# Performance work log

Measured on AMD Instinct MI355X. Metric: run time of the kernel, lower is better.

The kernel has to match this reference:

```python
import jax, jax.numpy as jnp
import numpy as np

DEPTH = 5  # init kwarg


def setup_inputs() -> dict:
    key = jax.random.key(0)
    ks = jax.random.split(key, 10)
    n_atoms, n_bonds, hidden, n_mols = 80000, 160001, 448, 4000
    ATOM_DIM, BOND_DIM = 38, 11
    inp = {
        "fatoms": jax.random.normal(ks[0], (n_atoms, ATOM_DIM), jnp.float32),
        "fbonds": jax.random.normal(ks[1], (n_bonds, ATOM_DIM + BOND_DIM), jnp.float32),
        "W_i": jax.random.normal(ks[2], (ATOM_DIM + BOND_DIM, hidden), jnp.float32) * 0.1,
        "W_h": jax.random.normal(ks[3], (hidden, hidden), jnp.float32) * 0.05,
        "W_o": jax.random.normal(ks[4], (ATOM_DIM + hidden, hidden), jnp.float32) * 0.05,
        "b_o": jax.random.normal(ks[5], (hidden,), jnp.float32),
        "agraph": jax.random.randint(ks[6], (n_atoms, 6), 0, n_bonds, jnp.int64),
        "bgraph": jax.random.randint(ks[7], (n_bonds, 6), 0, n_bonds, jnp.int64),
        "mol_idx": jnp.sort(jax.random.randint(ks[8], (n_atoms,), 0, n_mols, jnp.int64)),
        "n_mols": n_mols,
    }
    return inp


def reference(fatoms, fbonds, W_i, W_h, W_o, b_o, agraph, bgraph, mol_idx, n_mols):
    # binput: [n_bonds, hidden]
    binput = fbonds @ W_i
    message = jax.nn.relu(binput)
    for _ in range(DEPTH - 1):
        # padded-neighbor gather-sum over MAX_NB=6, then linear + relu
        nei = jnp.take(message, bgraph, axis=0).sum(axis=1)  # [n_bonds, hidden]
        message = jax.nn.relu(binput + nei @ W_h)
    # atom readout
    nei = jnp.take(message, agraph, axis=0).sum(axis=1)  # [n_atoms, hidden]
    ainput = jnp.concatenate([fatoms, nei], axis=1)
    atom_hiddens = jax.nn.relu(ainput @ W_o + b_o)
    # per-molecule mean pooling (scope -> segment ids)
    sums = jax.ops.segment_sum(atom_hiddens, mol_idx, num_segments=n_mols)
    counts = jax.ops.segment_sum(jnp.ones((atom_hiddens.shape[0],), atom_hiddens.dtype), mol_idx, num_segments=n_mols)
    return sums / jnp.maximum(counts, 1.0)[:, None]
```

## Files before the change

### kernel.cpp

```cpp
#include <hip/hip_runtime.h>

#define HIDDEN 448

typedef __attribute__((ext_vector_type(8))) short short8;
typedef __attribute__((ext_vector_type(4))) float f32x4;

__device__ __forceinline__ unsigned short f2bf(float f) {
    unsigned int u = __float_as_uint(f);
    u = (u + 0x7fffu + ((u >> 16) & 1u)) >> 16;
    return (unsigned short)u;
}
__device__ __forceinline__ float bf2f(unsigned short h) {
    return __uint_as_float(((unsigned int)h) << 16);
}
__device__ __forceinline__ unsigned int cvt_pk_bf16(float a, float b) {
    unsigned int r;
    asm("v_cvt_pk_bf16_f32 %0, %1, %2" : "=v"(r) : "v"(a), "v"(b));
    return r;
}
__device__ __forceinline__ void async16(void* lds, const void* g) {
    __builtin_amdgcn_global_load_lds(
        (const __attribute__((address_space(1))) unsigned int*)g,
        (__attribute__((address_space(3))) unsigned int*)lds, 16, 0, 0);
}

__global__ __launch_bounds__(256) void prep_wcat_kernel(
    const float* __restrict__ Wtop, int Ktop, const float* __restrict__ Wbot,
    unsigned short* __restrict__ out)
{
    const int idx = blockIdx.x * 256 + threadIdx.x;
    if (idx >= 448 * 512) return;
    const int n = idx >> 9, k = idx & 511;
    float v = 0.0f;
    if (k < Ktop) v = Wtop[k * HIDDEN + n];
    else if (k >= 64) v = Wbot[(k - 64) * HIDDEN + n];
    out[(size_t)n * 512 + (k ^ (((n >> 1) & 3) << 3))] = f2bf(v);
}

__global__ __launch_bounds__(256) void prep_apad_kernel(
    const float* __restrict__ A, int K, unsigned short* __restrict__ out,
    int Mreal, int total)
{
    const int idx = blockIdx.x * 256 + threadIdx.x;
    if (idx >= total) return;
    const int row = idx >> 6, k = idx & 63;
    const float v = (row < Mreal && k < K) ? A[(size_t)row * K + k] : 0.0f;
    out[(size_t)row * 64 + (k ^ (((row >> 1) & 3) << 3))] = f2bf(v);
}

template<int GRAPH, int OUTQ>
__global__ __launch_bounds__(512, 4) void gemm_mfma_kernel(
    const unsigned short* __restrict__ Apad,
    const unsigned char* __restrict__ Xq,
    const float* __restrict__ Xs,
    const int* __restrict__ graph,
    const unsigned short* __restrict__ BT,
    const float* __restrict__ bias,
    unsigned short* outh,
    unsigned char* __restrict__ outq,
    float* __restrict__ outs,
    int M, int nsteps)
{
    __shared__ __align__(16) unsigned char smem[37888];
    unsigned short* As = (unsigned short*)smem;
    unsigned short* Bs = (unsigned short*)(smem + 8192);
    float* rmaxbuf = (float*)(smem + 36864);

    const int tid = threadIdx.x, lane = tid & 63, wv = tid >> 6;
    const int row0 = blockIdx.x * 64;
    const int wrow = (wv & 1) * 32;
    const int wcol = (wv >> 1) * 112;
    const int rr = lane & 15, ch = lane >> 4;
    const int lrow = lane >> 2, lq = lane & 3;

    const int arow = tid >> 3, asub = tid & 7;
    const int ahh = asub >> 2, ac = asub & 3;
    const int awoff = arow * 64 + ahh * 32 + ((ac ^ ((arow >> 1) & 3)) << 3);

    int goff[6]; float gscl[6]; uint2 pf[6]; uint4 wreg;
    if (GRAPH) {
        const int grow = row0 + arow;
        const bool ok = grow < M;
        #pragma unroll
        for (int j = 0; j < 6; ++j) {
            const int gj = ok ? graph[(size_t)grow * 6 + j] : 0;
            goff[j] = gj * 448;
            gscl[j] = ok ? Xs[gj] : 0.0f;
        }
    }

    f32x4 acc[2][7] = {};

    for (int s = 0; s < nsteps; ++s) {
        if (GRAPH && s >= 2 && !(s & 1))
            *(uint4*)&As[awoff] = wreg;
        #pragma unroll
        for (int i = 0; i < 4; ++i) {
            const int t = wv + 8 * i;
            if (t < 28)
                async16(Bs + t * 512 + lane * 8,
                        BT + (size_t)(t * 16 + lrow) * 512 + s * 32 + lq * 8);
        }
        if (s == 0)
            async16(As + wv * 512 + lane * 8,
                    Apad + (size_t)(row0 + wv * 8) * 64 + lane * 8);
        __syncthreads();

        if (GRAPH && !(s & 1) && s <= 12) {
            const int pb = (s >> 1) * 64;
            #pragma unroll
            for (int j = 0; j < 6; ++j)
                pf[j] = *(const uint2*)(Xq + goff[j] + pb + asub * 8);
        }

        const int hoff = (s & 1) * 32;
        short8 av[2], bv[7];
        #pragma unroll
        for (int m = 0; m < 2; ++m) {
            const int r = wrow + m * 16 + rr;
            av[m] = *(const short8*)&As[r * 64 + hoff + ((ch ^ ((r >> 1) & 3)) << 3)];
        }
        #pragma unroll
        for (int n = 0; n < 7; ++n) {
            const int cl = wcol + n * 16 + rr;
            bv[n] = *(const short8*)&Bs[cl * 32 + ((ch ^ ((cl >> 1) & 3)) << 3)];
        }
        #pragma unroll
        for (int n = 0; n < 7; ++n)
            #pragma unroll
            for (int m = 0; m < 2; ++m)
                acc[m][n] = __builtin_amdgcn_mfma_f32_16x16x32_bf16(
                    av[m], bv[n], acc[m][n], 0, 0, 0);

        if (GRAPH && (s & 1) && s <= 13) {
            float a0 = 0, a1 = 0, a2 = 0, a3 = 0, a4 = 0, a5 = 0, a6 = 0, a7 = 0;
            #pragma unroll
            for (int j = 0; j < 6; ++j) {
                const uint2 b = pf[j];
                const float sc = gscl[j];
                a0 += (float)(b.x & 255u) * sc;
                a1 += (float)((b.x >> 8) & 255u) * sc;
                a2 += (float)((b.x >> 16) & 255u) * sc;
                a3 += (float)(b.x >> 24) * sc;
                a4 += (float)(b.y & 255u) * sc;
                a5 += (float)((b.y >> 8) & 255u) * sc;
                a6 += (float)((b.y >> 16) & 255u) * sc;
                a7 += (float)(b.y >> 24) * sc;
            }
            wreg.x = cvt_pk_bf16(a0, a1);
            wreg.y = cvt_pk_bf16(a2, a3);
            wreg.z = cvt_pk_bf16(a4, a5);
            wreg.w = cvt_pk_bf16(a6, a7);
        }
        __syncthreads();
    }

    const int r4 = ch << 2;

    if (OUTQ) {
        float rpm[2][4];
        #pragma unroll
        for (int m = 0; m < 2; ++m)
            #pragma unroll
            for (int j = 0; j < 4; ++j) {
                float mx = 0.0f;
                #pragma unroll
                for (int n = 0; n < 7; ++n) mx = fmaxf(mx, acc[m][n][j]);
                rpm[m][j] = mx;
            }
        #pragma unroll
        for (int off = 1; off < 16; off <<= 1)
            #pragma unroll
            for (int m = 0; m < 2; ++m)
                #pragma unroll
                for (int j = 0; j < 4; ++j)
                    rpm[m][j] = fmaxf(rpm[m][j], __shfl_xor(rpm[m][j], off));
        if (rr == 0)
            #pragma unroll
            for (int m = 0; m < 2; ++m)
                #pragma unroll
                for (int j = 0; j < 4; ++j)
                    rmaxbuf[(wrow + m * 16 + r4 + j) * 4 + (wv >> 1)] = rpm[m][j];
        __syncthreads();
        float inv[2][4];
        #pragma unroll
        for (int m = 0; m < 2; ++m)
            #pragma unroll
            for (int j = 0; j < 4; ++j) {
                const int rl = wrow + m * 16 + r4 + j;
                const float mx = fmaxf(fmaxf(rmaxbuf[rl * 4 + 0], rmaxbuf[rl * 4 + 1]),
                                       fmaxf(rmaxbuf[rl * 4 + 2], rmaxbuf[rl * 4 + 3]));
                inv[m][j] = (mx > 0.0f) ? (255.0f / mx) : 0.0f;
                if (wv < 2 && rr == 0 && row0 + rl < M)
                    outs[row0 + rl] = mx * (1.0f / 255.0f);
            }
        __syncthreads();
        unsigned char* q8 = smem;
        #pragma unroll
        for (int m = 0; m < 2; ++m)
            #pragma unroll
            for (int j = 0; j < 4; ++j) {
                const int rl = wrow + m * 16 + r4 + j;
                #pragma unroll
                for (int n = 0; n < 7; ++n) {
                    const float v = fmaxf(acc[m][n][j], 0.0f);
                    q8[rl * 448 + wcol + n * 16 + rr] =
                        (unsigned char)__float2uint_rn(fminf(v * inv[m][j], 255.0f));
                }
            }
        __syncthreads();
        #pragma unroll
        for (int i = 0; i < 4; ++i) {
            const int u = tid + 512 * i;
            if (u < 1792 && row0 + u / 28 < M)
                ((uint4*)(outq + (size_t)row0 * 448))[u] = ((const uint4*)q8)[u];
        }
    } else {
        #pragma unroll
        for (int n = 0; n < 7; ++n) {
            const int col = wcol + n * 16 + rr;
            const float bsv = bias ? bias[col] : 0.0f;
            #pragma unroll
            for (int m = 0; m < 2; ++m)
                #pragma unroll
                for (int j = 0; j < 4; ++j) {
                    const int row = row0 + wrow + m * 16 + r4 + j;
                    if (row < M)
                        outh[(size_t)row * HIDDEN + col] =
                            f2bf(fmaxf(acc[m][n][j] + bsv, 0.0f));
                }
        }
    }
}

__global__ void segmean_kernel(
    const unsigned short* __restrict__ ah, const int* __restrict__ mol_idx,
    float* __restrict__ out, int n_atoms)
{
    const int m = blockIdx.x;
    const int c = threadIdx.x;
    int l = 0, r = n_atoms;
    while (l < r) { const int mid = (l + r) >> 1; if (mol_idx[mid] < m) l = mid + 1; else r = mid; }
    const int start = l;
    r = n_atoms;
    while (l < r) { const int mid = (l + r) >> 1; if (mol_idx[mid] < m + 1) l = mid + 1; else r = mid; }
    const int end = l;
    float acc = 0.0f;
    for (int a = start; a < end; ++a) acc += bf2f(ah[(size_t)a * HIDDEN + c]);
    out[(size_t)m * HIDDEN + c] = acc / fmaxf((float)(end - start), 1.0f);
}

__global__ __launch_bounds__(256) void fill_kernel(float* __restrict__ out, int n, float val)
{
    const int i = blockIdx.x * 256 + threadIdx.x;
    if (i < n) out[i] = val;
}

extern "C" void kernel_launch(void* const* d_in, const int* in_sizes, int n_in,
                              void* d_out, int out_size, void* d_ws, size_t ws_size,
                              hipStream_t stream)
{
    const float* fatoms = (const float*)d_in[0];
    const float* fbonds = (const float*)d_in[1];
    const float* W_i    = (const float*)d_in[2];
    const float* W_h    = (const float*)d_in[3];
    const float* W_o    = (const float*)d_in[4];
    const float* b_o    = (const float*)d_in[5];
    const int*   agraph = (const int*)d_in[6];
    const int*   bgraph = (const int*)d_in[7];
    const int*   mol_idx= (const int*)d_in[8];

    const int n_atoms = in_sizes[0] / 38;
    const int n_bonds = in_sizes[1] / 49;
    const int n_mols  = out_size / HIDDEN;

    const int Mb_b = (n_bonds + 63) & ~63;
    const int Mb_a = (n_atoms + 63) & ~63;

    const size_t eW  = (size_t)448 * 512;
    const size_t eFb = (size_t)Mb_b * 64;
    const size_t eFa = (size_t)Mb_a * 64;
    const size_t eX  = (size_t)Mb_b * 448;

    const size_t need = 2 * eW * 2 + eFb * 2 + eFa * 2 +
                        2 * eX + 2 * (size_t)Mb_b * 4;

    const dim3 blk(256);

    if (ws_size >= need) {
        unsigned short* WhcatT  = (unsigned short*)d_ws;
        unsigned short* WocatT  = WhcatT + eW;
        unsigned short* fbondsP = WocatT + eW;
        unsigned short* fatomsP = fbondsP + eFb;
        unsigned char*  Xq0     = (unsigned char*)(fatomsP + eFa);
        unsigned char*  Xq1     = Xq0 + eX;
        float*          Xs0     = (float*)(Xq1 + eX);
        float*          Xs1     = Xs0 + Mb_b;

        const int wblocks = (448 * 512 + 255) / 256;
        hipLaunchKernelGGL(prep_wcat_kernel, dim3(wblocks), blk, 0, stream,
                           W_i, 49, W_h, WhcatT);
        hipLaunchKernelGGL(prep_wcat_kernel, dim3(wblocks), blk, 0, stream,
                           W_o, 38, W_o + 38 * HIDDEN, WocatT);
        hipLaunchKernelGGL(prep_apad_kernel, dim3(((int)eFb + 255) / 256), blk, 0, stream,
                           fbonds, 49, fbondsP, n_bonds, (int)eFb);
        hipLaunchKernelGGL(prep_apad_kernel, dim3(((int)eFa + 255) / 256), blk, 0, stream,
                           fatoms, 38, fatomsP, n_atoms, (int)eFa);

        const dim3 gB(Mb_b / 64), gA(Mb_a / 64), tpb(512);

        unsigned char* Xq[2] = {Xq0, Xq1};
        float*         Xs[2] = {Xs0, Xs1};

        hipLaunchKernelGGL((gemm_mfma_kernel<0, 1>), gB, tpb, 0, stream,
                           fbondsP, (const unsigned char*)nullptr, (const float*)nullptr,
                           (const int*)nullptr, WhcatT, (const float*)nullptr,
                           (unsigned short*)nullptr, Xq[0], Xs[0], n_bonds, 2);
        int p = 0;
        for (int it = 0; it < 4; ++it) {
            hipLaunchKernelGGL((gemm_mfma_kernel<1, 1>), gB, tpb, 0, stream,
                               fbondsP, Xq[p], Xs[p], bgraph, WhcatT,
                               (const float*)nullptr, (unsigned short*)nullptr,
                               Xq[p ^ 1], Xs[p ^ 1], n_bonds, 16);
            p ^= 1;
        }
        unsigned short* ah = (unsigned short*)Xq[p ^ 1];
        hipLaunchKernelGGL((gemm_mfma_kernel<1, 0>), gA, tpb, 0, stream,
                           fatomsP, Xq[p], Xs[p], agraph, WocatT, b_o,
                           ah, (unsigned char*)nullptr, (float*)nullptr, n_atoms, 16);
        hipLaunchKernelGGL(segmean_kernel, dim3(n_mols), dim3(HIDDEN), 0, stream,
                           ah, mol_idx, (float*)d_out, n_atoms);
    } else {
        const float val = -(float)((double)ws_size / (1024.0 * 1024.0));
        hipLaunchKernelGGL(fill_kernel, dim3((out_size + 255) / 256), blk, 0, stream,
                           (float*)d_out, out_size, val);
    }
}
```

Before: 1.014 ms.

## Fuse segment-mean pooling into readout GEMM epilogue via atomics

The atom readout GEMM epilogue now sums each thread's four rows per molecule and adds the result into the output with atomicAdd, instead of writing bf16 atom hiddens to memory. The segmean kernel becomes a simple normalization pass, and the output is zeroed with a memset first. The gather-reduce step is also moved from the end of an odd iteration to the start of the next even one, so the wreg carry register is no longer needed. This removes the intermediate write and re-read of the atom hidden states, at the cost of atomic contention and summation order that is no longer deterministic.

```diff
diff --git a/kernel.cpp b/kernel.cpp
--- a/kernel.cpp
+++ b/kernel.cpp
@@ -56,9 +56,10 @@
     const int* __restrict__ graph,
     const unsigned short* __restrict__ BT,
     const float* __restrict__ bias,
-    unsigned short* outh,
     unsigned char* __restrict__ outq,
     float* __restrict__ outs,
+    const int* __restrict__ molv,
+    float* __restrict__ dout,
     int M, int nsteps)
 {
     __shared__ __align__(16) unsigned char smem[37888];
@@ -75,9 +76,9 @@
 
     const int arow = tid >> 3, asub = tid & 7;
     const int ahh = asub >> 2, ac = asub & 3;
-    const int awoff = arow * 64 + ahh * 32 + ((ac ^ ((arow >> 1) & 3)) << 3);
-
-    int goff[6]; float gscl[6]; uint2 pf[6]; uint4 wreg;
+    const int awaddr = arow * 64 + ahh * 32 + ((ac ^ ((arow >> 1) & 3)) << 3);
+
+    int goff[6]; float gscl[6]; uint2 pf[6];
     if (GRAPH) {
         const int grow = row0 + arow;
         const bool ok = grow < M;
@@ -92,47 +93,7 @@
     f32x4 acc[2][7] = {};
 
     for (int s = 0; s < nsteps; ++s) {
-        if (GRAPH && s >= 2 && !(s & 1))
-            *(uint4*)&As[awoff] = wreg;
-        #pragma unroll
-        for (int i = 0; i < 4; ++i) {
-            const int t = wv + 8 * i;
-            if (t < 28)
-                async16(Bs + t * 512 + lane * 8,
-                        BT + (size_t)(t * 16 + lrow) * 512 + s * 32 + lq * 8);
-        }
-        if (s == 0)
-            async16(As + wv * 512 + lane * 8,
-                    Apad + (size_t)(row0 + wv * 8) * 64 + lane * 8);
-        __syncthreads();
-
-        if (GRAPH && !(s & 1) && s <= 12) {
-            const int pb = (s >> 1) * 64;
-            #pragma unroll
-            for (int j = 0; j < 6; ++j)
-                pf[j] = *(const uint2*)(Xq + goff[j] + pb + asub * 8);
-        }
-
-        const int hoff = (s & 1) * 32;
-        short8 av[2], bv[7];
-        #pragma unroll
-        for (int m = 0; m < 2; ++m) {
-            const int r = wrow + m * 16 + rr;
-            av[m] = *(const short8*)&As[r * 64 + hoff + ((ch ^ ((r >> 1) & 3)) << 3)];
-        }
-        #pragma unroll
-        for (int n = 0; n < 7; ++n) {
-            const int cl = wcol + n * 16 + rr;
-            bv[n] = *(const short8*)&Bs[cl * 32 + ((ch ^ ((cl >> 1) & 3)) << 3)];
-        }
-        #pragma unroll
-        for (int n = 0; n < 7; ++n)
-            #pragma unroll
-            for (int m = 0; m < 2; ++m)
-                acc[m][n] = __builtin_amdgcn_mfma_f32_16x16x32_bf16(
-                    av[m], bv[n], acc[m][n], 0, 0, 0);
-
-        if (GRAPH && (s & 1) && s <= 13) {
+        if (GRAPH && s >= 2 && !(s & 1)) {
             float a0 = 0, a1 = 0, a2 = 0, a3 = 0, a4 = 0, a5 = 0, a6 = 0, a7 = 0;
             #pragma unroll
             for (int j = 0; j < 6; ++j) {
@@ -147,11 +108,51 @@
                 a6 += (float)((b.y >> 16) & 255u) * sc;
                 a7 += (float)(b.y >> 24) * sc;
             }
-            wreg.x = cvt_pk_bf16(a0, a1);
-            wreg.y = cvt_pk_bf16(a2, a3);
-            wreg.z = cvt_pk_bf16(a4, a5);
-            wreg.w = cvt_pk_bf16(a6, a7);
-        }
+            uint4 w;
+            w.x = cvt_pk_bf16(a0, a1);
+            w.y = cvt_pk_bf16(a2, a3);
+            w.z = cvt_pk_bf16(a4, a5);
+            w.w = cvt_pk_bf16(a6, a7);
+            *(uint4*)&As[awaddr] = w;
+        }
+        #pragma unroll
+        for (int i = 0; i < 4; ++i) {
+            const int t = wv + 8 * i;
+            if (t < 28)
+                async16(Bs + t * 512 + lane * 8,
+                        BT + (size_t)(t * 16 + lrow) * 512 + s * 32 + lq * 8);
+        }
+        if (s == 0)
+            async16(As + wv * 512 + lane * 8,
+                    Apad + (size_t)(row0 + wv * 8) * 64 + lane * 8);
+        __syncthreads();
+
+        if (GRAPH && !(s & 1) && s <= 12) {
+            const int pb = (s >> 1) * 64;
+            #pragma unroll
+            for (int j = 0; j < 6; ++j)
+                pf[j] = *(const uint2*)(Xq + goff[j] + pb + asub * 8);
+        }
+
+        const int hoff = (s & 1) * 32;
+        short8 av[2], bv[7];
+        #pragma unroll
+        for (int m = 0; m < 2; ++m) {
+            const int r = wrow + m * 16 + rr;
+            av[m] = *(const short8*)&As[r * 64 + hoff + ((ch ^ ((r >> 1) & 3)) << 3)];
+        }
+        #pragma unroll
+        for (int n = 0; n < 7; ++n) {
+            const int cl = wcol + n * 16 + rr;
+            bv[n] = *(const short8*)&Bs[cl * 32 + ((ch ^ ((cl >> 1) & 3)) << 3)];
+        }
+        #pragma unroll
+        for (int n = 0; n < 7; ++n)
+            #pragma unroll
+            for (int m = 0; m < 2; ++m)
+                acc[m][n] = __builtin_amdgcn_mfma_f32_16x16x32_bf16(
+                    av[m], bv[n], acc[m][n], 0, 0, 0);
+
         __syncthreads();
     }
 
@@ -216,26 +217,45 @@
                 ((uint4*)(outq + (size_t)row0 * 448))[u] = ((const uint4*)q8)[u];
         }
     } else {
+        int mols[2][4];
+        #pragma unroll
+        for (int m = 0; m < 2; ++m)
+            #pragma unroll
+            for (int j = 0; j < 4; ++j) {
+                const int row = row0 + wrow + m * 16 + r4 + j;
+                mols[m][j] = (row < M) ? molv[row] : -1;
+            }
         #pragma unroll
         for (int n = 0; n < 7; ++n) {
             const int col = wcol + n * 16 + rr;
             const float bsv = bias ? bias[col] : 0.0f;
             #pragma unroll
-            for (int m = 0; m < 2; ++m)
+            for (int m = 0; m < 2; ++m) {
+                int curmol = -1;
+                float rs = 0.0f;
                 #pragma unroll
                 for (int j = 0; j < 4; ++j) {
-                    const int row = row0 + wrow + m * 16 + r4 + j;
-                    if (row < M)
-                        outh[(size_t)row * HIDDEN + col] =
-                            f2bf(fmaxf(acc[m][n][j] + bsv, 0.0f));
+                    if (mols[m][j] >= 0) {
+                        const float v = fmaxf(acc[m][n][j] + bsv, 0.0f);
+                        if (mols[m][j] != curmol) {
+                            if (curmol >= 0)
+                                atomicAdd(dout + (size_t)curmol * HIDDEN + col, rs);
+                            curmol = mols[m][j];
+                            rs = v;
+                        } else {
+                            rs += v;
+                        }
+                    }
                 }
+                if (curmol >= 0)
+                    atomicAdd(dout + (size_t)curmol * HIDDEN + col, rs);
+            }
         }
     }
 }
 
-__global__ void segmean_kernel(
-    const unsigned short* __restrict__ ah, const int* __restrict__ mol_idx,
-    float* __restrict__ out, int n_atoms)
+__global__ void norm_kernel(float* __restrict__ out,
+                            const int* __restrict__ mol_idx, int n_atoms)
 {
     const int m = blockIdx.x;
     const int c = threadIdx.x;
@@ -244,10 +264,7 @@
     const int start = l;
     r = n_atoms;
     while (l < r) { const int mid = (l + r) >> 1; if (mol_idx[mid] < m + 1) l = mid + 1; else r = mid; }
-    const int end = l;
-    float acc = 0.0f;
-    for (int a = start; a < end; ++a) acc += bf2f(ah[(size_t)a * HIDDEN + c]);
-    out[(size_t)m * HIDDEN + c] = acc / fmaxf((float)(end - start), 1.0f);
+    out[(size_t)m * HIDDEN + c] /= fmaxf((float)(l - start), 1.0f);
 }
 
 __global__ __launch_bounds__(256) void fill_kernel(float* __restrict__ out, int n, float val)
@@ -297,6 +314,8 @@
         float*          Xs0     = (float*)(Xq1 + eX);
         float*          Xs1     = Xs0 + Mb_b;
 
+        hipMemsetAsync(d_out, 0, (size_t)out_size * sizeof(float), stream);
+
         const int wblocks = (448 * 512 + 255) / 256;
         hipLaunchKernelGGL(prep_wcat_kernel, dim3(wblocks), blk, 0, stream,
                            W_i, 49, W_h, WhcatT);
@@ -315,21 +334,23 @@
         hipLaunchKernelGGL((gemm_mfma_kernel<0, 1>), gB, tpb, 0, stream,
                            fbondsP, (const unsigned char*)nullptr, (const float*)nullptr,
                            (const int*)nullptr, WhcatT, (const float*)nullptr,
-                           (unsigned short*)nullptr, Xq[0], Xs[0], n_bonds, 2);
+                           Xq[0], Xs[0], (const int*)nullptr, (float*)nullptr,
+                           n_bonds, 2);
         int p = 0;
         for (int it = 0; it < 4; ++it) {
             hipLaunchKernelGGL((gemm_mfma_kernel<1, 1>), gB, tpb, 0, stream,
                                fbondsP, Xq[p], Xs[p], bgraph, WhcatT,
-                               (const float*)nullptr, (unsigned short*)nullptr,
-                               Xq[p ^ 1], Xs[p ^ 1], n_bonds, 16);
+                               (const float*)nullptr,
+                               Xq[p ^ 1], Xs[p ^ 1], (const int*)nullptr,
+                               (float*)nullptr, n_bonds, 16);
             p ^= 1;
         }
-        unsigned short* ah = (unsigned short*)Xq[p ^ 1];
         hipLaunchKernelGGL((gemm_mfma_kernel<1, 0>), gA, tpb, 0, stream,
                            fatomsP, Xq[p], Xs[p], agraph, WocatT, b_o,
-                           ah, (unsigned char*)nullptr, (float*)nullptr, n_atoms, 16);
-        hipLaunchKernelGGL(segmean_kernel, dim3(n_mols), dim3(HIDDEN), 0, stream,
-                           ah, mol_idx, (float*)d_out, n_atoms);
+                           (unsigned char*)nullptr, (float*)nullptr,
+                           mol_idx, (float*)d_out, n_atoms, 16);
+        hipLaunchKernelGGL(norm_kernel, dim3(n_mols), dim3(HIDDEN), 0, stream,
+                           (float*)d_out, mol_idx, n_atoms);
     } else {
         const float val = -(float)((double)ws_size / (1024.0 * 1024.0));
         hipLaunchKernelGGL(fill_kernel, dim3((out_size + 255) / 256), blk, 0, stream,
```

Result: faster. 882.3 us (-13.0%).
